# Optimization experiments

Hardware: AMD Instinct MI355X
Metric: run time of the kernel (lower is better)

## Reference

```python
import jax, jax.numpy as jnp
import numpy as np

B, T, C = 4, 2048, 1024
H = 16
HS = C // H  # 64
FF = 4 * C
EPS = 1e-5


def setup_inputs() -> dict:
    key = jax.random.key(0)
    ks = jax.random.split(key, 12)
    s = lambda k, shape, fan: jax.random.normal(k, shape, jnp.float32) * (fan ** -0.5)
    return {
        "x": jax.random.normal(ks[0], (B, T, C), jnp.float32),
        "Wq": s(ks[1], (H, C, HS), C),
        "Wk": s(ks[2], (H, C, HS), C),
        "Wv": s(ks[3], (H, C, HS), C),
        "Wproj": s(ks[4], (C, C), C),
        "bproj": jnp.zeros((C,), jnp.float32),
        "W1": s(ks[5], (C, FF), C),
        "b1": jnp.zeros((FF,), jnp.float32),
        "W2": s(ks[6], (FF, C), FF),
        "b2": jnp.zeros((C,), jnp.float32),
        "g1": jnp.ones((C,), jnp.float32),
        "be1": jnp.zeros((C,), jnp.float32),
        "g2": jnp.ones((C,), jnp.float32),
        "be2": jnp.zeros((C,), jnp.float32),
    }


def _layernorm(x, g, b):
    mu = jnp.mean(x, axis=-1, keepdims=True)
    var = jnp.mean(jnp.square(x - mu), axis=-1, keepdims=True)
    return (x - mu) * jax.lax.rsqrt(var + EPS) * g + b


def reference(x, Wq, Wk, Wv, Wproj, bproj, W1, b1, W2, b2, g1, be1, g2, be2):
    # --- multi-head causal self-attention on ln1(x) ---
    h = _layernorm(x, g1, be1)                      # [B,T,C]
    q = jnp.einsum("btc,hcd->bhtd", h, Wq)
    k = jnp.einsum("btc,hcd->bhtd", h, Wk)
    v = jnp.einsum("btc,hcd->bhtd", h, Wv)
    scores = jnp.einsum("bhtd,bhsd->bhts", q, k) * (HS ** -0.5)  # [B,H,T,T]
    causal = jnp.tril(jnp.ones((T, T), bool))
    scores = jnp.where(causal, scores, -jnp.inf)
    wei = jax.nn.softmax(scores, axis=-1)
    attn = jnp.einsum("bhts,bhsd->bhtd", wei, v)    # [B,H,T,HS]
    attn = attn.transpose(0, 2, 1, 3).reshape(B, T, C)  # concat heads
    x = x + attn @ Wproj + bproj
    # --- feed-forward on ln2(x) ---
    h2 = _layernorm(x, g2, be2)
    x = x + jax.nn.relu(h2 @ W1 + b1) @ W2 + b2
    return x
```

## Files before the change

### kernel.cpp

```cpp
#include <hip/hip_runtime.h>
#include <hip/hip_bf16.h>
#include <stdint.h>


typedef unsigned short u16;
typedef __bf16 bf16x8 __attribute__((ext_vector_type(8)));
typedef float f32x4 __attribute__((ext_vector_type(4)));
typedef float f32x16 __attribute__((ext_vector_type(16)));

#define MFMA16(a, b, c) __builtin_amdgcn_mfma_f32_16x16x32_bf16((a), (b), (c), 0, 0, 0)
#define MFMA32(a, b, c) __builtin_amdgcn_mfma_f32_32x32x16_bf16((a), (b), (c), 0, 0, 0)

__device__ __forceinline__ u16 f2bf(float f) {
  __hip_bfloat16 h = __float2bfloat16(f);
  return __builtin_bit_cast(u16, h);
}

__device__ __forceinline__ uint32_t cvtpk(float lo, float hi_) {
  uint32_t r;
  asm("v_cvt_pk_bf16_f32 %0, %1, %2" : "=v"(r) : "v"(lo), "v"(hi_));
  return r;
}

__device__ __forceinline__ void pl32swap(uint32_t& a, uint32_t& b) {
  asm("v_permlane32_swap_b32 %0, %1" : "+v"(a), "+v"(b));
}

__device__ __forceinline__ void gload16(const void* g, void* l) {
  __builtin_amdgcn_global_load_lds(
      (__attribute__((address_space(1))) void*)g,
      (__attribute__((address_space(3))) void*)l, 16, 0, 0);
}

__global__ __launch_bounds__(256) void ln_kernel(
    const float* __restrict__ x, const float* __restrict__ g,
    const float* __restrict__ be, u16* __restrict__ out) {
  const int row = blockIdx.x;
  const int tid = threadIdx.x;
  const float4 v = reinterpret_cast<const float4*>(x + (size_t)row * 1024)[tid];
  float s = v.x + v.y + v.z + v.w;
  float s2 = v.x * v.x + v.y * v.y + v.z * v.z + v.w * v.w;
#pragma unroll
  for (int off = 1; off < 64; off <<= 1) {
    s += __shfl_xor(s, off);
    s2 += __shfl_xor(s2, off);
  }
  __shared__ float red[8];
  const int wid = tid >> 6;
  if ((tid & 63) == 0) { red[wid] = s; red[4 + wid] = s2; }
  __syncthreads();
  s = red[0] + red[1] + red[2] + red[3];
  s2 = red[4] + red[5] + red[6] + red[7];
  const float mu = s * (1.0f / 1024.0f);
  const float rstd = rsqrtf(s2 * (1.0f / 1024.0f) - mu * mu + 1e-5f);
  const float4 gv = reinterpret_cast<const float4*>(g)[tid];
  const float4 bv = reinterpret_cast<const float4*>(be)[tid];
  ushort4 o;
  o.x = f2bf((v.x - mu) * rstd * gv.x + bv.x);
  o.y = f2bf((v.y - mu) * rstd * gv.y + bv.y);
  o.z = f2bf((v.z - mu) * rstd * gv.z + bv.z);
  o.w = f2bf((v.w - mu) * rstd * gv.w + bv.w);
  *reinterpret_cast<ushort4*>(out + (size_t)row * 1024 + tid * 4) = o;
}

__global__ __launch_bounds__(256) void tcvt(
    const float* __restrict__ src, u16* __restrict__ dst,
    int R, int C, size_t sstride, size_t dstride) {
  src += (size_t)blockIdx.z * sstride;
  dst += (size_t)blockIdx.z * dstride;
  __shared__ float t[64][65];
  const int r0 = blockIdx.x * 64, c0 = blockIdx.y * 64;
  const int tid = threadIdx.x;
  const int cc = tid & 63, rr = tid >> 6;
#pragma unroll
  for (int p = 0; p < 16; ++p) {
    const int r = rr + p * 4;
    t[r][cc] = src[(size_t)(r0 + r) * C + c0 + cc];
  }
  __syncthreads();
#pragma unroll
  for (int p = 0; p < 16; ++p) {
    const int c = rr + p * 4;
    dst[(size_t)(c0 + c) * R + r0 + cc] = f2bf(t[cc][c]);
  }
}

constexpr int EPI_QKV = 0;
constexpr int EPI_RES = 1;
constexpr int EPI_RELU = 2;

template <int EPI>
__global__ __launch_bounds__(512) void gemm256(
    const u16* __restrict__ A, const u16* __restrict__ Bt,
    int M, int N, int K, int NBN,
    u16* outB, float* outF, const float* bias) {
  __shared__ u16 sA[2][256 * 64] __attribute__((aligned(16)));
  __shared__ u16 sB[2][256 * 64] __attribute__((aligned(16)));
  const int tid = threadIdx.x;
  const int lane = tid & 63, wid = tid >> 6;
  const int wr = wid >> 2, wc = wid & 3;
  const int l16 = lane & 15, lg = lane >> 4;
  const int nwg = gridDim.x;
  const int wgid = (blockIdx.x & 7) * (nwg >> 3) + (blockIdx.x >> 3);
  const int bm = wgid / NBN, bn = wgid % NBN;
  const size_t rowA = (size_t)bm * 256;
  const size_t rowB = (size_t)bn * 256;
  const int nkt = K >> 6;

  f32x4 acc[8][4];
#pragma unroll
  for (int m = 0; m < 8; ++m)
#pragma unroll
    for (int n = 0; n < 4; ++n) {
      acc[m][n][0] = 0.f; acc[m][n][1] = 0.f; acc[m][n][2] = 0.f; acc[m][n][3] = 0.f;
    }

  auto stageA = [&](int kt, int h) {
    if (kt >= nkt) return;
    const int k0 = kt << 6;
    char* base = (char*)&sA[kt & 1][h * 8192];
#pragma unroll
    for (int it = 0; it < 2; ++it) {
      const int f = tid + it * 512;
      const int r = f >> 3, c = f & 7;
      gload16(A + (rowA + h * 128 + r) * K + k0 + ((c ^ (r & 7)) << 3), base + f * 16);
    }
  };
  auto stageB = [&](int kt, int h) {
    if (kt >= nkt) return;
    const int k0 = kt << 6;
    char* base = (char*)&sB[kt & 1][h * 8192];
#pragma unroll
    for (int it = 0; it < 2; ++it) {
      const int f = tid + it * 512;
      const int r = f >> 3, c = f & 7;
      gload16(Bt + (rowB + h * 128 + r) * K + k0 + ((c ^ (r & 7)) << 3), base + f * 16);
    }
  };

  stageA(0, 0); stageB(0, 0); stageA(0, 1); stageB(0, 1);
  stageB(1, 0); stageA(1, 0);
  asm volatile("s_waitcnt vmcnt(4)" ::: "memory");
  __builtin_amdgcn_s_barrier();
  asm volatile("" ::: "memory");

  bf16x8 a[4][2], b[4][2];
  for (int kt = 0; kt < nkt; ++kt) {
    const u16* bufA = &sA[kt & 1][0];
    const u16* bufB = &sB[kt & 1][0];
#pragma unroll
    for (int m = 0; m < 4; ++m)
#pragma unroll
      for (int kk = 0; kk < 2; ++kk) {
        const int r = wr * 128 + m * 16 + l16;
        a[m][kk] = *reinterpret_cast<const bf16x8*>(bufA + r * 64 + (((kk * 4 + lg) ^ (r & 7)) << 3));
      }
#pragma unroll
    for (int n = 0; n < 2; ++n)
#pragma unroll
      for (int kk = 0; kk < 2; ++kk) {
        const int r = wc * 64 + n * 16 + l16;
        b[n][kk] = *reinterpret_cast<const bf16x8*>(bufB + r * 64 + (((kk * 4 + lg) ^ (r & 7)) << 3));
      }
    stageB(kt + 1, 1);
    __builtin_amdgcn_s_barrier();
    asm volatile("s_waitcnt lgkmcnt(0)" ::: "memory");
    __builtin_amdgcn_s_setprio(1);
#pragma unroll
    for (int kk = 0; kk < 2; ++kk)
#pragma unroll
      for (int m = 0; m < 4; ++m)
#pragma unroll
        for (int n = 0; n < 2; ++n)
          acc[m][n] = MFMA16(a[m][kk], b[n][kk], acc[m][n]);
    __builtin_amdgcn_s_setprio(0);
    __builtin_amdgcn_s_barrier();
    asm volatile("" ::: "memory");
#pragma unroll
    for (int n = 2; n < 4; ++n)
#pragma unroll
      for (int kk = 0; kk < 2; ++kk) {
        const int r = wc * 64 + n * 16 + l16;
        b[n][kk] = *reinterpret_cast<const bf16x8*>(bufB + r * 64 + (((kk * 4 + lg) ^ (r & 7)) << 3));
      }
    stageA(kt + 1, 1);
    __builtin_amdgcn_s_barrier();
    asm volatile("s_waitcnt lgkmcnt(0)" ::: "memory");
    __builtin_amdgcn_s_setprio(1);
#pragma unroll
    for (int kk = 0; kk < 2; ++kk)
#pragma unroll
      for (int m = 0; m < 4; ++m)
#pragma unroll
        for (int n = 2; n < 4; ++n)
          acc[m][n] = MFMA16(a[m][kk], b[n][kk], acc[m][n]);
    __builtin_amdgcn_s_setprio(0);
    __builtin_amdgcn_s_barrier();
    asm volatile("" ::: "memory");
#pragma unroll
    for (int m = 0; m < 4; ++m)
#pragma unroll
      for (int kk = 0; kk < 2; ++kk) {
        const int r = wr * 128 + 64 + m * 16 + l16;
        a[m][kk] = *reinterpret_cast<const bf16x8*>(bufA + r * 64 + (((kk * 4 + lg) ^ (r & 7)) << 3));
      }
    stageB(kt + 2, 0);
    __builtin_amdgcn_s_barrier();
    asm volatile("s_waitcnt lgkmcnt(0)" ::: "memory");
    __builtin_amdgcn_s_setprio(1);
#pragma unroll
    for (int kk = 0; kk < 2; ++kk)
#pragma unroll
      for (int m = 0; m < 4; ++m)
#pragma unroll
        for (int n = 2; n < 4; ++n)
          acc[4 + m][n] = MFMA16(a[m][kk], b[n][kk], acc[4 + m][n]);
    __builtin_amdgcn_s_setprio(0);
    __builtin_amdgcn_s_barrier();
    asm volatile("" ::: "memory");
    stageA(kt + 2, 0);
    __builtin_amdgcn_s_setprio(1);
#pragma unroll
    for (int kk = 0; kk < 2; ++kk)
#pragma unroll
      for (int m = 0; m < 4; ++m)
#pragma unroll
        for (int n = 0; n < 2; ++n)
          acc[4 + m][n] = MFMA16(a[m][kk], b[n][kk], acc[4 + m][n]);
    __builtin_amdgcn_s_setprio(0);
    if (kt + 2 < nkt) {
      asm volatile("s_waitcnt vmcnt(4)" ::: "memory");
    } else {
      asm volatile("s_waitcnt vmcnt(0)" ::: "memory");
    }
    __builtin_amdgcn_s_barrier();
    asm volatile("" ::: "memory");
  }

#pragma unroll
  for (int m = 0; m < 8; ++m)
#pragma unroll
    for (int n = 0; n < 4; ++n)
#pragma unroll
      for (int ii = 0; ii < 4; ++ii) {
        const int gi = bm * 256 + wr * 128 + m * 16 + lg * 4 + ii;
        const int gj = bn * 256 + wc * 64 + n * 16 + l16;
        const float val = acc[m][n][ii];
        if constexpr (EPI == EPI_RELU) {
          const float bv = val + bias[gj];
          outB[(size_t)gi * N + gj] = f2bf(bv > 0.f ? bv : 0.f);
        }
      }
}

template <int EPI>
__global__ __launch_bounds__(512) void gemm128(
    const u16* __restrict__ A, const u16* __restrict__ Bt,
    int M, int N, int K, int NBN,
    u16* outB, float* outF, const float* bias, const float* res) {
  __shared__ u16 sA[2][128 * 64] __attribute__((aligned(16)));
  __shared__ u16 sB[2][256 * 64] __attribute__((aligned(16)));
  const int tid = threadIdx.x;
  const int lane = tid & 63, wid = tid >> 6;
  const int wr = wid >> 2, wc = wid & 3;
  const int l16 = lane & 15, lg = lane >> 4;
  const int nwg = gridDim.x;
  const int wgid = (blockIdx.x & 7) * (nwg >> 3) + (blockIdx.x >> 3);
  const int bm = wgid / NBN, bn = wgid % NBN;
  const size_t rowA = (size_t)bm * 128;
  const size_t rowB = (size_t)bn * 256;
  const int nkt = K >> 6;

  f32x4 acc[4][4];
#pragma unroll
  for (int m = 0; m < 4; ++m)
#pragma unroll
    for (int n = 0; n < 4; ++n) {
      acc[m][n][0] = 0.f; acc[m][n][1] = 0.f; acc[m][n][2] = 0.f; acc[m][n][3] = 0.f;
    }

  auto stageA = [&](int kt, int h) {
    if (kt >= nkt) return;
    const int k0 = kt << 6;
    char* base = (char*)&sA[kt & 1][h * 4096];
    const int r = tid >> 3, c = tid & 7;
    gload16(A + (rowA + h * 64 + r) * K + k0 + ((c ^ (r & 7)) << 3), base + tid * 16);
  };
  auto stageB = [&](int kt, int h) {
    if (kt >= nkt) return;
    const int k0 = kt << 6;
    char* base = (char*)&sB[kt & 1][h * 8192];
#pragma unroll
    for (int it = 0; it < 2; ++it) {
      const int f = tid + it * 512;
      const int r = f >> 3, c = f & 7;
      gload16(Bt + (rowB + h * 128 + r) * K + k0 + ((c ^ (r & 7)) << 3), base + f * 16);
    }
  };

  stageA(0, 0); stageB(0, 0); stageA(0, 1); stageB(0, 1);
  stageB(1, 0); stageA(1, 0);
  asm volatile("s_waitcnt vmcnt(3)" ::: "memory");
  __builtin_amdgcn_s_barrier();
  asm volatile("" ::: "memory");

  bf16x8 a[2][2], b[4][2];
  for (int kt = 0; kt < nkt; ++kt) {
    const u16* bufA = &sA[kt & 1][0];
    const u16* bufB = &sB[kt & 1][0];
#pragma unroll
    for (int m = 0; m < 2; ++m)
#pragma unroll
      for (int kk = 0; kk < 2; ++kk) {
        const int r = wr * 64 + m * 16 + l16;
        a[m][kk] = *reinterpret_cast<const bf16x8*>(bufA + r * 64 + (((kk * 4 + lg) ^ (r & 7)) << 3));
      }
#pragma unroll
    for (int n = 0; n < 2; ++n)
#pragma unroll
      for (int kk = 0; kk < 2; ++kk) {
        const int r = wc * 64 + n * 16 + l16;
        b[n][kk] = *reinterpret_cast<const bf16x8*>(bufB + r * 64 + (((kk * 4 + lg) ^ (r & 7)) << 3));
      }
    stageB(kt + 1, 1);
    __builtin_amdgcn_s_barrier();
    asm volatile("s_waitcnt lgkmcnt(0)" ::: "memory");
    __builtin_amdgcn_s_setprio(1);
#pragma unroll
    for (int kk = 0; kk < 2; ++kk)
#pragma unroll
      for (int m = 0; m < 2; ++m)
#pragma unroll
        for (int n = 0; n < 2; ++n)
          acc[m][n] = MFMA16(a[m][kk], b[n][kk], acc[m][n]);
    __builtin_amdgcn_s_setprio(0);
    __builtin_amdgcn_s_barrier();
    asm volatile("" ::: "memory");
#pragma unroll
    for (int n = 2; n < 4; ++n)
#pragma unroll
      for (int kk = 0; kk < 2; ++kk) {
        const int r = wc * 64 + n * 16 + l16;
        b[n][kk] = *reinterpret_cast<const bf16x8*>(bufB + r * 64 + (((kk * 4 + lg) ^ (r & 7)) << 3));
      }
    stageA(kt + 1, 1);
    __builtin_amdgcn_s_barrier();
    asm volatile("s_waitcnt lgkmcnt(0)" ::: "memory");
    __builtin_amdgcn_s_setprio(1);
#pragma unroll
    for (int kk = 0; kk < 2; ++kk)
#pragma unroll
      for (int m = 0; m < 2; ++m)
#pragma unroll
        for (int n = 2; n < 4; ++n)
          acc[m][n] = MFMA16(a[m][kk], b[n][kk], acc[m][n]);
    __builtin_amdgcn_s_setprio(0);
    __builtin_amdgcn_s_barrier();
    asm volatile("" ::: "memory");
#pragma unroll
    for (int m = 0; m < 2; ++m)
#pragma unroll
      for (int kk = 0; kk < 2; ++kk) {
        const int r = wr * 64 + (m + 2) * 16 + l16;
        a[m][kk] = *reinterpret_cast<const bf16x8*>(bufA + r * 64 + (((kk * 4 + lg) ^ (r & 7)) << 3));
      }
    stageB(kt + 2, 0);
    __builtin_amdgcn_s_barrier();
    asm volatile("s_waitcnt lgkmcnt(0)" ::: "memory");
    __builtin_amdgcn_s_setprio(1);
#pragma unroll
    for (int kk = 0; kk < 2; ++kk)
#pragma unroll
      for (int m = 0; m < 2; ++m)
#pragma unroll
        for (int n = 2; n < 4; ++n)
          acc[2 + m][n] = MFMA16(a[m][kk], b[n][kk], acc[2 + m][n]);
    __builtin_amdgcn_s_setprio(0);
    __builtin_amdgcn_s_barrier();
    asm volatile("" ::: "memory");
    stageA(kt + 2, 0);
    __builtin_amdgcn_s_setprio(1);
#pragma unroll
    for (int kk = 0; kk < 2; ++kk)
#pragma unroll
      for (int m = 0; m < 2; ++m)
#pragma unroll
        for (int n = 0; n < 2; ++n)
          acc[2 + m][n] = MFMA16(a[m][kk], b[n][kk], acc[2 + m][n]);
    __builtin_amdgcn_s_setprio(0);
    if (kt + 2 < nkt) {
      asm volatile("s_waitcnt vmcnt(3)" ::: "memory");
    } else {
      asm volatile("s_waitcnt vmcnt(0)" ::: "memory");
    }
    __builtin_amdgcn_s_barrier();
    asm volatile("" ::: "memory");
  }

#pragma unroll
  for (int m = 0; m < 4; ++m)
#pragma unroll
    for (int n = 0; n < 4; ++n)
#pragma unroll
      for (int ii = 0; ii < 4; ++ii) {
        const int gi = bm * 128 + wr * 64 + m * 16 + lg * 4 + ii;
        const int gj = bn * 256 + wc * 64 + n * 16 + l16;
        const float val = acc[m][n][ii];
        if constexpr (EPI == EPI_QKV) {
          const int sel = gj >> 10;
          const int hh = (gj >> 6) & 15;
          const int dd = gj & 63;
          const int bb = gi >> 11, tt = gi & 2047;
          const float sv = (sel == 0) ? val * 0.1803368801f : val;
          outB[(size_t)sel * 8388608 + ((size_t)(bb * 16 + hh) * 2048 + tt) * 64 + dd] = f2bf(sv);
        } else if constexpr (EPI == EPI_RES) {
          const size_t idx = (size_t)gi * N + gj;
          outF[idx] = val + bias[gj] + res[idx];
        }
      }
}

__global__ __launch_bounds__(256, 3) void attn_kernel(
    const u16* __restrict__ q, const u16* __restrict__ k,
    const u16* __restrict__ v, u16* __restrict__ o) {
  const int bid = blockIdx.x;
  const int bh = (bid & 7) * 8 + ((bid >> 3) & 7);
  const int qt = 15 - (bid >> 6);
  const int tid = threadIdx.x;
  const int lane = tid & 63, wid = tid >> 6;
  const int l32 = lane & 31, hi = lane >> 5;
  const u16* qb = q + (size_t)bh * (2048 * 64);
  const u16* kb = k + (size_t)bh * (2048 * 64);
  const u16* vb = v + (size_t)bh * (2048 * 64);
  const int q0 = qt * 128;
  const int qrow = q0 + wid * 32 + l32;

  __shared__ u16 sK[2][64 * 64] __attribute__((aligned(16)));
  __shared__ u16 sVt[2][64 * 72] __attribute__((aligned(16)));

  bf16x8 bq[4];
#pragma unroll
  for (int s = 0; s < 4; ++s)
    bq[s] = *reinterpret_cast<const bf16x8*>(qb + (size_t)qrow * 64 + s * 16 + hi * 8);

  f32x16 oacc[2];
#pragma unroll
  for (int r = 0; r < 16; ++r) { oacc[0][r] = 0.f; oacc[1][r] = 0.f; }
  float mi = -1e30f, li = 0.f;

  uint4 vr0, vr1;

  auto stageK = [&](int s0, int buf) {
#pragma unroll
    for (int it = 0; it < 2; ++it) {
      const int f = tid + it * 256;
      const int r = f >> 3, c = f & 7;
      gload16(kb + (size_t)(s0 + r) * 64 + (size_t)((c ^ (r & 7)) * 8),
              (char*)&sK[buf][0] + it * 4096 + wid * 1024);
    }
  };
  auto loadV = [&](int s0) {
    const int kvp = tid & 31;
    const int c8 = tid >> 5;
    vr0 = *reinterpret_cast<const uint4*>(vb + (size_t)(s0 + 2 * kvp) * 64 + c8 * 8);
    vr1 = *reinterpret_cast<const uint4*>(vb + (size_t)(s0 + 2 * kvp + 1) * 64 + c8 * 8);
  };
  auto writeV = [&](int buf) {
    const int kvp = tid & 31;
    const int c8 = tid >> 5;
    const u16* e0 = reinterpret_cast<const u16*>(&vr0);
    const u16* e1 = reinterpret_cast<const u16*>(&vr1);
    u16* base = &sVt[buf][0];
#pragma unroll
    for (int j = 0; j < 8; ++j) {
      const int d = c8 * 8 + j;
      *reinterpret_cast<uint32_t*>(base + d * 72 + 2 * kvp) =
          (uint32_t)e0[j] | ((uint32_t)e1[j] << 16);
    }
  };

  const int nst = 2 * qt + 2;
  stageK(0, 0);
  loadV(0);
  asm volatile("s_waitcnt vmcnt(0)" ::: "memory");
  writeV(0);
  __syncthreads();

  int cur = 0;
  for (int ks = 0; ks < nst; ++ks) {
    const int s0 = ks * 64;
    const int nxt = cur ^ 1;
    if (ks + 1 < nst) { stageK(s0 + 64, nxt); loadV(s0 + 64); }

    f32x16 st[2];
#pragma unroll
    for (int r = 0; r < 16; ++r) { st[0][r] = 0.f; st[1][r] = 0.f; }
#pragma unroll
    for (int t = 0; t < 2; ++t) {
      const int row = t * 32 + l32;
      const int rx = row & 7;
#pragma unroll
      for (int s = 0; s < 4; ++s) {
        bf16x8 ak = *reinterpret_cast<const bf16x8*>(
            &sK[cur][0] + row * 64 + (((s * 2 + hi) ^ rx) << 3));
        st[t] = MFMA32(ak, bq[s], st[t]);
      }
    }

    if (ks >= 2 * qt) {
#pragma unroll
      for (int t = 0; t < 2; ++t)
#pragma unroll
        for (int a = 0; a < 4; ++a)
#pragma unroll
          for (int c2 = 0; c2 < 4; ++c2) {
            const int kvg = s0 + t * 32 + a * 8 + hi * 4 + c2;
            if (kvg > qrow) st[t][a * 4 + c2] = -1e30f;
          }
    }

    float pm = -3e38f;
#pragma unroll
    for (int t = 0; t < 2; ++t)
#pragma unroll
      for (int r = 0; r < 16; ++r) pm = fmaxf(pm, st[t][r]);
    pm = fmaxf(pm, __shfl_xor(pm, 32));
    if (__any(pm > mi)) {
      const float mn = fmaxf(mi, pm);
      const float al = exp2f(mi - mn);
      mi = mn;
      li *= al;
#pragma unroll
      for (int dt = 0; dt < 2; ++dt)
#pragma unroll
        for (int r = 0; r < 16; ++r) oacc[dt][r] *= al;
    }
    float rs = 0.f;
#pragma unroll
    for (int t = 0; t < 2; ++t)
#pragma unroll
      for (int r = 0; r < 16; ++r) {
        const float p = exp2f(st[t][r] - mi);
        st[t][r] = p;
        rs += p;
      }
    rs += __shfl_xor(rs, 32);
    li += rs;

    uint32_t W[2][4][2];
#pragma unroll
    for (int t = 0; t < 2; ++t)
#pragma unroll
      for (int a = 0; a < 4; ++a) {
        W[t][a][0] = cvtpk(st[t][a * 4 + 0], st[t][a * 4 + 1]);
        W[t][a][1] = cvtpk(st[t][a * 4 + 2], st[t][a * 4 + 3]);
      }
#pragma unroll
    for (int ks2 = 0; ks2 < 4; ++ks2) {
      const int t = ks2 >> 1;
      uint32_t A0 = W[t][(2 * ks2) & 3][0], B0 = W[t][(2 * ks2 + 1) & 3][0];
      uint32_t A1 = W[t][(2 * ks2) & 3][1], B1 = W[t][(2 * ks2 + 1) & 3][1];
      pl32swap(A0, B0);
      pl32swap(A1, B1);
      union { uint32_t w[4]; bf16x8 v; } bp;
      bp.w[0] = A0; bp.w[1] = A1; bp.w[2] = B0; bp.w[3] = B1;
#pragma unroll
      for (int dt = 0; dt < 2; ++dt) {
        bf16x8 av = *reinterpret_cast<const bf16x8*>(
            &sVt[cur][0] + (dt * 32 + l32) * 72 + ks2 * 16 + hi * 8);
        oacc[dt] = MFMA32(av, bp.v, oacc[dt]);
      }
    }

    if (ks + 1 < nst) {
      asm volatile("s_waitcnt vmcnt(0)" ::: "memory");
      writeV(nxt);
      __syncthreads();
    }
    cur = nxt;
  }

  const int bb = bh >> 4, hh = bh & 15;
  const float rli = 1.0f / li;
  const size_t rowo = (size_t)(bb * 2048 + qrow) * 1024;
#pragma unroll
  for (int dt = 0; dt < 2; ++dt)
#pragma unroll
    for (int a = 0; a < 4; ++a) {
      ushort4 pk;
      pk.x = f2bf(oacc[dt][a * 4 + 0] * rli);
      pk.y = f2bf(oacc[dt][a * 4 + 1] * rli);
      pk.z = f2bf(oacc[dt][a * 4 + 2] * rli);
      pk.w = f2bf(oacc[dt][a * 4 + 3] * rli);
      *reinterpret_cast<ushort4*>(o + rowo + hh * 64 + dt * 32 + a * 8 + hi * 4) = pk;
    }
}

extern "C" void kernel_launch(void* const* d_in, const int* in_sizes, int n_in,
                              void* d_out, int out_size, void* d_ws, size_t ws_size,
                              hipStream_t stream) {
  const float* x = (const float*)d_in[0];
  const float* Wq = (const float*)d_in[1];
  const float* Wk = (const float*)d_in[2];
  const float* Wv = (const float*)d_in[3];
  const float* Wproj = (const float*)d_in[4];
  const float* bproj = (const float*)d_in[5];
  const float* W1 = (const float*)d_in[6];
  const float* b1 = (const float*)d_in[7];
  const float* W2 = (const float*)d_in[8];
  const float* b2 = (const float*)d_in[9];
  const float* g1 = (const float*)d_in[10];
  const float* be1 = (const float*)d_in[11];
  const float* g2 = (const float*)d_in[12];
  const float* be2 = (const float*)d_in[13];
  float* out = (float*)d_out;

  char* ws = (char*)d_ws;
  const size_t MB16 = 16777216ull;
  u16* hb = (u16*)(ws);
  u16* qkv = (u16*)(ws + MB16);
  u16* qp = qkv;
  u16* kp = qkv + 8388608;
  u16* vp = qkv + 2 * 8388608;
  u16* ab = (u16*)(ws + 4 * MB16);
  u16* f1 = qkv;
  u16* wqkvt = (u16*)(ws + 5 * MB16);
  u16* wprojt = wqkvt + 3145728;
  u16* w1t = wprojt + 1048576;
  u16* w2t = w1t + 4194304;

  dim3 blk(256);
  tcvt<<<dim3(16, 1, 16), blk, 0, stream>>>(Wq, wqkvt, 1024, 64, 65536, 65536);
  tcvt<<<dim3(16, 1, 16), blk, 0, stream>>>(Wk, wqkvt + 1048576, 1024, 64, 65536, 65536);
  tcvt<<<dim3(16, 1, 16), blk, 0, stream>>>(Wv, wqkvt + 2097152, 1024, 64, 65536, 65536);
  tcvt<<<dim3(16, 16, 1), blk, 0, stream>>>(Wproj, wprojt, 1024, 1024, 0, 0);
  tcvt<<<dim3(16, 64, 1), blk, 0, stream>>>(W1, w1t, 1024, 4096, 0, 0);
  tcvt<<<dim3(64, 16, 1), blk, 0, stream>>>(W2, w2t, 4096, 1024, 0, 0);

  ln_kernel<<<8192, blk, 0, stream>>>(x, g1, be1, hb);
  gemm128<EPI_QKV><<<768, 512, 0, stream>>>(hb, wqkvt, 8192, 3072, 1024, 12,
                                            qkv, nullptr, nullptr, nullptr);
  attn_kernel<<<1024, blk, 0, stream>>>(qp, kp, vp, ab);
  gemm128<EPI_RES><<<256, 512, 0, stream>>>(ab, wprojt, 8192, 1024, 1024, 4,
                                            nullptr, out, bproj, x);
  ln_kernel<<<8192, blk, 0, stream>>>(out, g2, be2, hb);
  gemm256<EPI_RELU><<<512, 512, 0, stream>>>(hb, w1t, 8192, 4096, 1024, 16,
                                             f1, nullptr, b1);
  gemm128<EPI_RES><<<256, 512, 0, stream>>>(f1, w2t, 8192, 1024, 4096, 4,
                                            nullptr, out, b2, out);
}
```

Measured before the change: 407.1 us.

## Use 256x256 tiles for QKV GEMM and split-K FF2 GEMM with combine kernel

Moves the QKV projection from the 128x256 GEMM to the 256x256 GEMM, which halves the workgroup count and raises per-tile data reuse. The FF2 GEMM (K=4096) now runs as a 2-way split-K on 256x256 tiles and writes bf16 partial sums into reused workspace buffers. A new elementwise kernel adds the two partials, the bias and the residual into the fp32 output. This trades larger tiles and better load balance for an extra launch, extra memory traffic for the partials, and bf16 rounding of the partial sums.

```diff
diff --git a/kernel.cpp b/kernel.cpp
--- a/kernel.cpp
+++ b/kernel.cpp
@@ -14,6 +14,11 @@
 __device__ __forceinline__ u16 f2bf(float f) {
   __hip_bfloat16 h = __float2bfloat16(f);
   return __builtin_bit_cast(u16, h);
+}
+
+__device__ __forceinline__ float bf2f(u16 u) {
+  uint32_t t = (uint32_t)u << 16;
+  return __builtin_bit_cast(float, t);
 }
 
 __device__ __forceinline__ uint32_t cvtpk(float lo, float hi_) {
@@ -85,15 +90,41 @@
   }
 }
 
+__global__ __launch_bounds__(256) void ff2_combine(
+    const u16* __restrict__ p0, const u16* __restrict__ p1,
+    const float* __restrict__ b2, float* __restrict__ out) {
+  const size_t base = ((size_t)blockIdx.x * 256 + threadIdx.x) * 8;
+  const uint4 a0 = *reinterpret_cast<const uint4*>(p0 + base);
+  const uint4 a1 = *reinterpret_cast<const uint4*>(p1 + base);
+  const u16* e0 = reinterpret_cast<const u16*>(&a0);
+  const u16* e1 = reinterpret_cast<const u16*>(&a1);
+  const int c = (int)(base & 1023);
+  const float4 bv0 = *reinterpret_cast<const float4*>(b2 + c);
+  const float4 bv1 = *reinterpret_cast<const float4*>(b2 + c + 4);
+  float4 o0 = *reinterpret_cast<const float4*>(out + base);
+  float4 o1 = *reinterpret_cast<const float4*>(out + base + 4);
+  o0.x += bf2f(e0[0]) + bf2f(e1[0]) + bv0.x;
+  o0.y += bf2f(e0[1]) + bf2f(e1[1]) + bv0.y;
+  o0.z += bf2f(e0[2]) + bf2f(e1[2]) + bv0.z;
+  o0.w += bf2f(e0[3]) + bf2f(e1[3]) + bv0.w;
+  o1.x += bf2f(e0[4]) + bf2f(e1[4]) + bv1.x;
+  o1.y += bf2f(e0[5]) + bf2f(e1[5]) + bv1.y;
+  o1.z += bf2f(e0[6]) + bf2f(e1[6]) + bv1.z;
+  o1.w += bf2f(e0[7]) + bf2f(e1[7]) + bv1.w;
+  *reinterpret_cast<float4*>(out + base) = o0;
+  *reinterpret_cast<float4*>(out + base + 4) = o1;
+}
+
 constexpr int EPI_QKV = 0;
 constexpr int EPI_RES = 1;
 constexpr int EPI_RELU = 2;
+constexpr int EPI_PART = 3;
 
 template <int EPI>
 __global__ __launch_bounds__(512) void gemm256(
     const u16* __restrict__ A, const u16* __restrict__ Bt,
-    int M, int N, int K, int NBN,
-    u16* outB, float* outF, const float* bias) {
+    int M, int N, int Kloop, int Kstride, int NBN, int SPLIT,
+    u16* outB, u16* outB2, float* outF, const float* bias) {
   __shared__ u16 sA[2][256 * 64] __attribute__((aligned(16)));
   __shared__ u16 sB[2][256 * 64] __attribute__((aligned(16)));
   const int tid = threadIdx.x;
@@ -102,10 +133,15 @@
   const int l16 = lane & 15, lg = lane >> 4;
   const int nwg = gridDim.x;
   const int wgid = (blockIdx.x & 7) * (nwg >> 3) + (blockIdx.x >> 3);
-  const int bm = wgid / NBN, bn = wgid % NBN;
+  int wg = wgid, ks = 0;
+  if (SPLIT) { ks = wg & 1; wg >>= 1; }
+  const int bm = wg / NBN, bn = wg % NBN;
+  const u16* Ap = A + (size_t)ks * Kloop;
+  const u16* Btp = Bt + (size_t)ks * Kloop;
+  u16* outp = (SPLIT && ks) ? outB2 : outB;
   const size_t rowA = (size_t)bm * 256;
   const size_t rowB = (size_t)bn * 256;
-  const int nkt = K >> 6;
+  const int nkt = Kloop >> 6;
 
   f32x4 acc[8][4];
 #pragma unroll
@@ -123,7 +159,7 @@
     for (int it = 0; it < 2; ++it) {
       const int f = tid + it * 512;
       const int r = f >> 3, c = f & 7;
-      gload16(A + (rowA + h * 128 + r) * K + k0 + ((c ^ (r & 7)) << 3), base + f * 16);
+      gload16(Ap + (rowA + h * 128 + r) * Kstride + k0 + ((c ^ (r & 7)) << 3), base + f * 16);
     }
   };
   auto stageB = [&](int kt, int h) {
@@ -134,7 +170,7 @@
     for (int it = 0; it < 2; ++it) {
       const int f = tid + it * 512;
       const int r = f >> 3, c = f & 7;
-      gload16(Bt + (rowB + h * 128 + r) * K + k0 + ((c ^ (r & 7)) << 3), base + f * 16);
+      gload16(Btp + (rowB + h * 128 + r) * Kstride + k0 + ((c ^ (r & 7)) << 3), base + f * 16);
     }
   };
 
@@ -246,9 +282,18 @@
         const int gi = bm * 256 + wr * 128 + m * 16 + lg * 4 + ii;
         const int gj = bn * 256 + wc * 64 + n * 16 + l16;
         const float val = acc[m][n][ii];
-        if constexpr (EPI == EPI_RELU) {
+        if constexpr (EPI == EPI_QKV) {
+          const int sel = gj >> 10;
+          const int hh = (gj >> 6) & 15;
+          const int dd = gj & 63;
+          const int bb = gi >> 11, tt = gi & 2047;
+          const float sv = (sel == 0) ? val * 0.1803368801f : val;
+          outB[(size_t)sel * 8388608 + ((size_t)(bb * 16 + hh) * 2048 + tt) * 64 + dd] = f2bf(sv);
+        } else if constexpr (EPI == EPI_RELU) {
           const float bv = val + bias[gj];
           outB[(size_t)gi * N + gj] = f2bf(bv > 0.f ? bv : 0.f);
+        } else if constexpr (EPI == EPI_PART) {
+          outp[(size_t)gi * N + gj] = f2bf(val);
         }
       }
 }
@@ -406,14 +451,7 @@
         const int gi = bm * 128 + wr * 64 + m * 16 + lg * 4 + ii;
         const int gj = bn * 256 + wc * 64 + n * 16 + l16;
         const float val = acc[m][n][ii];
-        if constexpr (EPI == EPI_QKV) {
-          const int sel = gj >> 10;
-          const int hh = (gj >> 6) & 15;
-          const int dd = gj & 63;
-          const int bb = gi >> 11, tt = gi & 2047;
-          const float sv = (sel == 0) ? val * 0.1803368801f : val;
-          outB[(size_t)sel * 8388608 + ((size_t)(bb * 16 + hh) * 2048 + tt) * 64 + dd] = f2bf(sv);
-        } else if constexpr (EPI == EPI_RES) {
+        if constexpr (EPI == EPI_RES) {
           const size_t idx = (size_t)gi * N + gj;
           outF[idx] = val + bias[gj] + res[idx];
         }
@@ -628,6 +666,8 @@
   u16* wprojt = wqkvt + 3145728;
   u16* w1t = wprojt + 1048576;
   u16* w2t = w1t + 4194304;
+  u16* p0 = hb;
+  u16* p1 = wqkvt;
 
   dim3 blk(256);
   tcvt<<<dim3(16, 1, 16), blk, 0, stream>>>(Wq, wqkvt, 1024, 64, 65536, 65536);
@@ -638,14 +678,15 @@
   tcvt<<<dim3(64, 16, 1), blk, 0, stream>>>(W2, w2t, 4096, 1024, 0, 0);
 
   ln_kernel<<<8192, blk, 0, stream>>>(x, g1, be1, hb);
-  gemm128<EPI_QKV><<<768, 512, 0, stream>>>(hb, wqkvt, 8192, 3072, 1024, 12,
+  gemm256<EPI_QKV><<<384, 512, 0, stream>>>(hb, wqkvt, 8192, 3072, 1024, 1024, 12, 0,
                                             qkv, nullptr, nullptr, nullptr);
   attn_kernel<<<1024, blk, 0, stream>>>(qp, kp, vp, ab);
   gemm128<EPI_RES><<<256, 512, 0, stream>>>(ab, wprojt, 8192, 1024, 1024, 4,
                                             nullptr, out, bproj, x);
   ln_kernel<<<8192, blk, 0, stream>>>(out, g2, be2, hb);
-  gemm256<EPI_RELU><<<512, 512, 0, stream>>>(hb, w1t, 8192, 4096, 1024, 16,
-                                             f1, nullptr, b1);
-  gemm128<EPI_RES><<<256, 512, 0, stream>>>(f1, w2t, 8192, 1024, 4096, 4,
-                                            nullptr, out, b2, out);
-}
+  gemm256<EPI_RELU><<<512, 512, 0, stream>>>(hb, w1t, 8192, 4096, 1024, 1024, 16, 0,
+                                             f1, nullptr, nullptr, b1);
+  gemm256<EPI_PART><<<256, 512, 0, stream>>>(f1, w2t, 8192, 1024, 2048, 4096, 4, 1,
+                                             p0, p1, nullptr, nullptr);
+  ff2_combine<<<4096, blk, 0, stream>>>(p0, p1, b2, out);
+}
```

New measurement: 373.8 us. 8.2% less time.
